# Kernel optimization log

Hardware: AMD Instinct MI355X
Metric: run time of the kernel (lower is better)

## Reference

```python
import jax, jax.numpy as jnp
import numpy as np

HEADS = 8
KD = 64  # key_dim
VD = 64  # value_dim


def _conv1x1(W, b, x):
    # 1x1 conv == per-pixel matmul over channels. W: [out, in], x: [b, in, h, w]
    return jnp.einsum('oc,bchw->bohw', W, x) + b[:, None, None]


def setup_inputs() -> dict:
    key = jax.random.key(0)
    ks = jax.random.split(key, 9)
    B, C, H, W = 4, 128, 128, 128
    s = 0.02
    return {
        'x':  jax.random.normal(ks[0], (B, C, H, W), jnp.float32),
        'Wq': jax.random.normal(ks[1], (KD * HEADS, C), jnp.float32) * s,
        'bq': jax.random.normal(ks[2], (KD * HEADS,), jnp.float32) * s,
        'Wk': jax.random.normal(ks[3], (KD * HEADS, C), jnp.float32) * s,
        'bk': jax.random.normal(ks[4], (KD * HEADS,), jnp.float32) * s,
        'Wv': jax.random.normal(ks[5], (VD * HEADS, C), jnp.float32) * s,
        'bv': jax.random.normal(ks[6], (VD * HEADS,), jnp.float32) * s,
        'Wo': jax.random.normal(ks[7], (C, VD * HEADS), jnp.float32) * s,
        'bo': jax.random.normal(ks[8], (C,), jnp.float32) * s,
    }


def reference(x, Wq, bq, Wk, bk, Wv, bv, Wo, bo):
    B, C, H, W = x.shape
    n = H * W
    scale = KD ** -0.25
    # projections -> [b, heads, dim, n]
    q = _conv1x1(Wq, bq, x).reshape(B, HEADS, KD, n) * scale
    k = _conv1x1(Wk, bk, x).reshape(B, HEADS, KD, n) * scale
    v = _conv1x1(Wv, bv, x).reshape(B, HEADS, VD, n)
    # linear attention: softmax k over tokens (n), softmax q over key dim (d)
    k = jax.nn.softmax(k, axis=-1)
    q = jax.nn.softmax(q, axis=-2)
    ctx = jnp.einsum('bhdn,bhen->bhde', k, v)   # [b, h, kd, vd] small context
    out = jnp.einsum('bhdn,bhde->bhen', q, ctx)  # [b, h, vd, n]
    out = out.reshape(B, HEADS * VD, H, W)
    return _conv1x1(Wo, bo, out)
```

## Files before the change

### kernel.cpp

```cpp
#include <hip/hip_runtime.h>

typedef unsigned short u16;
typedef __bf16 bf16x8 __attribute__((ext_vector_type(8)));
typedef float f32x4 __attribute__((ext_vector_type(4)));

#define N_ 16384
#define SCALE 0.35355339059327379f

__device__ __forceinline__ u16 f2bf(float f){
  union { float f; unsigned int i; } v; v.f = f;
  unsigned int b = v.i;
  return (u16)((b + 0x7FFFu + ((b >> 16) & 1u)) >> 16);
}
__device__ __forceinline__ unsigned int cvtpk(float a, float b){
  unsigned int r;
  asm("v_cvt_pk_bf16_f32 %0, %1, %2" : "=v"(r) : "v"(a), "v"(b));
  return r;
}

__global__ __launch_bounds__(256) void pconvx(const float* __restrict__ x,
    u16* __restrict__ xt, const float* __restrict__ Wq,
    const float* __restrict__ bq, const float* __restrict__ Wk,
    const float* __restrict__ bk, const float* __restrict__ Wv,
    const float* __restrict__ bv, u16* __restrict__ wkvf, u16* __restrict__ wqf,
    float* __restrict__ bkv, float* __restrict__ bqs){
  const int tid = threadIdx.x;
  const int bid = blockIdx.x;
  if (bid < 512){
    const int b = bid >> 7;
    const int kq = tid >> 6;
    const int t0 = (bid & 127) * 128 + 2 * (tid & 63);
    const float* xp = x + (size_t)(b * 128 + kq * 32) * N_ + t0;
    u16* dst = xt + (size_t)(b * N_ + t0) * 128;
#pragma unroll
    for (int gi = 0; gi < 4; gi++){
      float2 v[8];
#pragma unroll
      for (int j = 0; j < 8; j++)
        v[j] = *(const float2*)(xp + (size_t)(gi * 8 + j) * N_);
      const int g = kq * 4 + gi;
      {
        uint4 o;
        o.x = cvtpk(v[0].x, v[1].x); o.y = cvtpk(v[2].x, v[3].x);
        o.z = cvtpk(v[4].x, v[5].x); o.w = cvtpk(v[6].x, v[7].x);
        *(uint4*)(dst + ((g ^ (t0 & 15)) * 8)) = o;
      }
      {
        uint4 o;
        o.x = cvtpk(v[0].y, v[1].y); o.y = cvtpk(v[2].y, v[3].y);
        o.z = cvtpk(v[4].y, v[5].y); o.w = cvtpk(v[6].y, v[7].y);
        const int t = t0 + 1;
        *(uint4*)(dst + 128 + ((g ^ (t & 15)) * 8)) = o;
      }
    }
    return;
  }
  const int T = (bid - 512) * 256 + tid;
  if (T < 1024){
    int jj = T & 127, h = T >> 7;
    bkv[T] = (jj < 64) ? SCALE * bk[h * 64 + jj] : bv[h * 64 + jj - 64];
  } else if (T < 1536){
    bqs[T - 1024] = SCALE * bq[T - 1024];
  }
  const float* src; float sc; u16* dst;
  if (T < 16384){
    int l = T & 63, f = T >> 6;
    int ks = f & 3, jt = (f >> 2) & 7, h = f >> 5;
    int jj = 16 * jt + (l & 15);
    int k0 = ks * 32 + (l >> 4) * 8;
    if (jj < 64){ src = Wk + (size_t)(h * 64 + jj) * 128 + k0; sc = SCALE; }
    else        { src = Wv + (size_t)(h * 64 + jj - 64) * 128 + k0; sc = 1.f; }
    dst = wkvf + (size_t)f * 512 + l * 8;
  } else {
    int T2 = T - 16384;
    int l = T2 & 63, f = T2 >> 6;
    int ks = f & 3, dt = (f >> 2) & 3, h = f >> 4;
    int d = 16 * dt + (l & 15);
    int k0 = ks * 32 + (l >> 4) * 8;
    src = Wq + (size_t)(h * 64 + d) * 128 + k0; sc = SCALE;
    dst = wqf + (size_t)f * 512 + l * 8;
  }
  float4 a = *(const float4*)src, c = *(const float4*)(src + 4);
  ushort4 o0, o1;
  o0.x = f2bf(sc * a.x); o0.y = f2bf(sc * a.y); o0.z = f2bf(sc * a.z); o0.w = f2bf(sc * a.w);
  o1.x = f2bf(sc * c.x); o1.y = f2bf(sc * c.y); o1.z = f2bf(sc * c.z); o1.w = f2bf(sc * c.w);
  *(ushort4*)dst = o0; *(ushort4*)(dst + 4) = o1;
}

__global__ __launch_bounds__(256, 2) void kvctx(const u16* __restrict__ xt,
    const u16* __restrict__ wkvf, const float* __restrict__ bkv,
    float* __restrict__ pctx, float* __restrict__ prs){
  __shared__ u16 smem[32768];
  const int tid = threadIdx.x;
  const int chunk = blockIdx.x, h = blockIdx.y, b = blockIdx.z;
  const int w = tid >> 6, l = tid & 63, r15 = l & 15, q = l >> 4;
  const int th = w & 1, jh = w >> 1;

  bf16x8 wf[4][4];
#pragma unroll
  for (int ni = 0; ni < 4; ni++)
#pragma unroll
    for (int ks = 0; ks < 4; ks++)
      wf[ni][ks] = *(const bf16x8*)(wkvf +
          (size_t)((h * 8 + 4 * jh + ni) * 4 + ks) * 512 + l * 8);
  float barr[4];
#pragma unroll
  for (int ni = 0; ni < 4; ni++)
    barr[ni] = bkv[h * 128 + jh * 64 + 16 * ni + r15];

  const size_t tok0 = (size_t)b * N_ + chunk * 512;
  const char* gbase = (const char*)(xt + tok0 * 128);
  u16* sekv = smem + 16384;

#define STAGE(sub_)                                                            \
  {                                                                            \
    const char* gs = gbase + (size_t)(sub_)*32768 + w * 8192 + l * 16;         \
    char* ls = (char*)smem + w * 8192;                                         \
    _Pragma("unroll")                                                          \
    for (int p = 0; p < 8; p++)                                                \
      __builtin_amdgcn_global_load_lds(                                        \
          (const __attribute__((address_space(1))) void*)(gs + p * 1024),      \
          (__attribute__((address_space(3))) void*)(ls + p * 1024), 16, 0, 0); \
  }

  STAGE(0);
  __syncthreads();

  f32x4 acc2[4][4] = {};
  float rs[4] = {0.f, 0.f, 0.f, 0.f};

  for (int sub = 0; sub < 4; sub++){
    f32x4 acc1[4][4] = {};
#pragma unroll
    for (int ks = 0; ks < 4; ks++){
      bf16x8 xa[4];
#pragma unroll
      for (int mi = 0; mi < 4; mi++){
        int t = th * 64 + 16 * mi + r15;
        xa[mi] = *(const bf16x8*)&smem[t * 128 + (((ks * 4 + q) ^ r15) * 8)];
      }
#pragma unroll
      for (int mi = 0; mi < 4; mi++)
#pragma unroll
        for (int ni = 0; ni < 4; ni++)
          acc1[mi][ni] = __builtin_amdgcn_mfma_f32_16x16x32_bf16(
              xa[mi], wf[ni][ks], acc1[mi][ni], 0, 0, 0);
    }
    asm volatile("s_waitcnt lgkmcnt(0)" ::: "memory");
    __builtin_amdgcn_s_barrier();
    if (sub < 3) STAGE(sub + 1);
#pragma unroll
    for (int ni = 0; ni < 4; ni++){
      const float bb = barr[ni];
      const int j = jh * 64 + 16 * ni + r15;
      float ps = 0.f;
#pragma unroll
      for (int mi = 0; mi < 4; mi++){
        float vals[4];
#pragma unroll
        for (int r = 0; r < 4; r++) vals[r] = acc1[mi][ni][r] + bb;
        if (jh == 0){
#pragma unroll
          for (int r = 0; r < 4; r++){ vals[r] = __expf(vals[r]); ps += vals[r]; }
        }
        uint2 pk;
        pk.x = cvtpk(vals[0], vals[1]);
        pk.y = cvtpk(vals[2], vals[3]);
        int g8 = 16 * th + 4 * mi + q;
        int g8s = g8 ^ (2 * r15);
        *(uint2*)&sekv[j * 128 + g8s * 4] = pk;
      }
      if (jh == 0){
        ps += __shfl_xor(ps, 16); ps += __shfl_xor(ps, 32);
        rs[ni] += ps;
      }
    }
    asm volatile("s_waitcnt lgkmcnt(0)" ::: "memory");
    __builtin_amdgcn_s_barrier();
    {
      bf16x8 ka[4], va[4];
      const int g8s = (8 * w + 2 * q) ^ (2 * r15);
#pragma unroll
      for (int mi2 = 0; mi2 < 4; mi2++){
        int d = 16 * mi2 + r15;
        ka[mi2] = *(const bf16x8*)&sekv[d * 128 + g8s * 4];
      }
#pragma unroll
      for (int ni2 = 0; ni2 < 4; ni2++){
        int e = 16 * ni2 + r15;
        va[ni2] = *(const bf16x8*)&sekv[(64 + e) * 128 + g8s * 4];
      }
#pragma unroll
      for (int mi2 = 0; mi2 < 4; mi2++)
#pragma unroll
        for (int ni2 = 0; ni2 < 4; ni2++)
          acc2[mi2][ni2] = __builtin_amdgcn_mfma_f32_16x16x32_bf16(
              ka[mi2], va[ni2], acc2[mi2][ni2], 0, 0, 0);
    }
    __syncthreads();
  }
#undef STAGE
  float* fb = (float*)smem;
#pragma unroll
  for (int mi2 = 0; mi2 < 4; mi2++)
#pragma unroll
    for (int ni2 = 0; ni2 < 4; ni2++)
#pragma unroll
      for (int r = 0; r < 4; r++){
        int d = 16 * mi2 + 4 * q + r, e = 16 * ni2 + r15;
        fb[w * 4096 + d * 64 + e] = acc2[mi2][ni2][r];
      }
  __syncthreads();
  {
    float* dst = pctx + ((size_t)((b * 8 + h) * 32 + chunk)) * 4096 + tid * 16;
#pragma unroll
    for (int i = 0; i < 4; i++){
      int o = tid * 16 + 4 * i;
      float4 a = *(const float4*)(fb + o);
      float4 c = *(const float4*)(fb + 4096 + o);
      float4 d = *(const float4*)(fb + 8192 + o);
      float4 e = *(const float4*)(fb + 12288 + o);
      float4 s;
      s.x = a.x + c.x + d.x + e.x; s.y = a.y + c.y + d.y + e.y;
      s.z = a.z + c.z + d.z + e.z; s.w = a.w + c.w + d.w + e.w;
      *(float4*)(dst + 4 * i) = s;
    }
  }
  if (jh == 0 && q == 0){
    float* rb = prs + ((size_t)((b * 8 + h) * 32 + chunk)) * 128 + th * 64;
#pragma unroll
    for (int ni = 0; ni < 4; ni++) rb[16 * ni + r15] = rs[ni];
  }
}

__global__ __launch_bounds__(256) void redmker(const float* __restrict__ pctx,
    const float* __restrict__ prs, const float* __restrict__ Wo,
    u16* __restrict__ mtf){
  __shared__ float ctxh8[8][68];
  __shared__ float woht[64][132];
  __shared__ float rsh[8];
  const int tid = threadIdx.x;
  const int bh = blockIdx.x, s = blockIdx.y;
  const int h = bh & 7;
  {
    const int e4 = tid & 15, r0 = tid >> 4;
#pragma unroll
    for (int p = 0; p < 8; p++){
      int c = r0 + p * 16;
      float4 v = *(const float4*)(Wo + (size_t)c * 512 + h * 64 + 4 * e4);
      woht[4 * e4 + 0][c] = v.x; woht[4 * e4 + 1][c] = v.y;
      woht[4 * e4 + 2][c] = v.z; woht[4 * e4 + 3][c] = v.w;
    }
  }
  {
    const float* base = pctx + (size_t)bh * 131072 + s * 512 + tid * 2;
    float2 a = {0.f, 0.f};
#pragma unroll 4
    for (int c = 0; c < 32; c++){
      float2 v = *(const float2*)(base + c * 4096);
      a.x += v.x; a.y += v.y;
    }
    const int i = tid * 2;
    ctxh8[i >> 6][i & 63] = a.x;
    ctxh8[(i + 1) >> 6][(i + 1) & 63] = a.y;
  }
  {
    const int dl = tid >> 5, c = tid & 31;
    const int dg = s * 8 + dl;
    const float* rb = prs + (size_t)bh * 4096 + c * 128;
    float v = rb[dg] + rb[64 + dg];
    v += __shfl_xor(v, 1);  v += __shfl_xor(v, 2);
    v += __shfl_xor(v, 4);  v += __shfl_xor(v, 8);
    v += __shfl_xor(v, 16);
    if (c == 0) rsh[dl] = v;
  }
  __syncthreads();
  const int dl = tid >> 5, c0 = (tid & 31) * 4;
  const int d = s * 8 + dl;
  const float inv = 1.f / rsh[dl];
  float acc[4] = {0.f, 0.f, 0.f, 0.f};
  for (int e = 0; e < 64; e++){
    float cv = ctxh8[dl][e];
#pragma unroll
    for (int j = 0; j < 4; j++) acc[j] += cv * woht[e][c0 + j];
  }
  const int ks = d >> 5, lq = ((d >> 3) & 3) << 4, el = d & 7;
#pragma unroll
  for (int j = 0; j < 4; j++){
    int c = c0 + j;
    mtf[((size_t)(bh * 8 + (c >> 4)) * 2 + ks) * 512 + ((c & 15) | lq) * 8 + el]
        = f2bf(inv * acc[j]);
  }
}

__global__ __launch_bounds__(256, 3) void qout(const u16* __restrict__ xt,
    const u16* __restrict__ wqf, const float* __restrict__ bqs,
    const u16* __restrict__ mtf, const float* __restrict__ bo,
    float* __restrict__ out){
  __shared__ u16 smP[4][16 * 64];
  const int tid = threadIdx.x;
  const int tt = blockIdx.x, b = blockIdx.y;
  const int w = tid >> 6, l = tid & 63, r15 = l & 15, q = l >> 4;
  const int t0 = tt * 64;
  const int m7 = 2 * (r15 & 7);
  const int t = t0 + w * 16 + r15;

  bf16x8 xb[4];
#pragma unroll
  for (int ks = 0; ks < 4; ks++)
    xb[ks] = *(const bf16x8*)(xt + (size_t)(b * N_ + t) * 128 +
                              (((ks * 4 + q) ^ r15) * 8));

  u16* sp = smP[w];
  f32x4 acc3[8] = {};
  for (int h = 0; h < 8; h++){
    float bq_[4][4];
#pragma unroll
    for (int mi = 0; mi < 4; mi++){
      float4 v = *(const float4*)(bqs + h * 64 + 16 * mi + 4 * q);
      bq_[mi][0] = v.x; bq_[mi][1] = v.y; bq_[mi][2] = v.z; bq_[mi][3] = v.w;
    }
    f32x4 acc1[4] = {};
#pragma unroll
    for (int ks = 0; ks < 4; ks++){
      bf16x8 wqv[4];
#pragma unroll
      for (int mi = 0; mi < 4; mi++)
        wqv[mi] = *(const bf16x8*)(wqf +
            (size_t)((h * 4 + mi) * 4 + ks) * 512 + l * 8);
#pragma unroll
      for (int mi = 0; mi < 4; mi++)
        acc1[mi] = __builtin_amdgcn_mfma_f32_16x16x32_bf16(
            wqv[mi], xb[ks], acc1[mi], 0, 0, 0);
    }
    bf16x8 mfA[4], mfB[4];
#pragma unroll
    for (int mm = 0; mm < 4; mm++)
      mfA[mm] = *(const bf16x8*)(mtf +
          ((size_t)((b * 8 + h) * 8 + mm) * 2 + 0) * 512 + l * 8);
#pragma unroll
    for (int mm = 0; mm < 4; mm++)
      mfB[mm] = *(const bf16x8*)(mtf +
          ((size_t)((b * 8 + h) * 8 + 4 + mm) * 2 + 0) * 512 + l * 8);
    {
      float ps = 0.f;
#pragma unroll
      for (int mi = 0; mi < 4; mi++)
#pragma unroll
        for (int r = 0; r < 4; r++){
          float e = __expf(acc1[mi][r] + bq_[mi][r]);
          acc1[mi][r] = e; ps += e;
        }
      ps += __shfl_xor(ps, 16); ps += __shfl_xor(ps, 32);
      const float ci = 1.f / ps;
#pragma unroll
      for (int mi = 0; mi < 4; mi++){
        uint2 pk;
        pk.x = cvtpk(acc1[mi][0] * ci, acc1[mi][1] * ci);
        pk.y = cvtpk(acc1[mi][2] * ci, acc1[mi][3] * ci);
        int g8s = (4 * mi + q) ^ m7;
        *(uint2*)&sp[r15 * 64 + g8s * 4] = pk;
      }
    }
    bf16x8 pb0 = *(const bf16x8*)&sp[r15 * 64 + (((2 * q) ^ m7) * 4)];
    bf16x8 pb1 = *(const bf16x8*)&sp[r15 * 64 + (((8 + 2 * q) ^ m7) * 4)];
#pragma unroll
    for (int mm = 0; mm < 4; mm++)
      acc3[mm] = __builtin_amdgcn_mfma_f32_16x16x32_bf16(
          mfA[mm], pb0, acc3[mm], 0, 0, 0);
#pragma unroll
    for (int mm = 0; mm < 4; mm++)
      mfA[mm] = *(const bf16x8*)(mtf +
          ((size_t)((b * 8 + h) * 8 + mm) * 2 + 1) * 512 + l * 8);
#pragma unroll
    for (int mm = 0; mm < 4; mm++)
      acc3[4 + mm] = __builtin_amdgcn_mfma_f32_16x16x32_bf16(
          mfB[mm], pb0, acc3[4 + mm], 0, 0, 0);
#pragma unroll
    for (int mm = 0; mm < 4; mm++)
      mfB[mm] = *(const bf16x8*)(mtf +
          ((size_t)((b * 8 + h) * 8 + 4 + mm) * 2 + 1) * 512 + l * 8);
#pragma unroll
    for (int mm = 0; mm < 4; mm++)
      acc3[mm] = __builtin_amdgcn_mfma_f32_16x16x32_bf16(
          mfA[mm], pb1, acc3[mm], 0, 0, 0);
#pragma unroll
    for (int mm = 0; mm < 4; mm++)
      acc3[4 + mm] = __builtin_amdgcn_mfma_f32_16x16x32_bf16(
          mfB[mm], pb1, acc3[4 + mm], 0, 0, 0);
  }
#pragma unroll
  for (int mi = 0; mi < 8; mi++){
    float4 bv = *(const float4*)(bo + 16 * mi + 4 * q);
    float bs[4] = {bv.x, bv.y, bv.z, bv.w};
#pragma unroll
    for (int r = 0; r < 4; r++){
      int c = 16 * mi + 4 * q + r;
      out[(size_t)(b * 128 + c) * N_ + t] = acc3[mi][r] + bs[r];
    }
  }
}

extern "C" void kernel_launch(void* const* d_in, const int* in_sizes, int n_in,
                              void* d_out, int out_size, void* d_ws, size_t ws_size,
                              hipStream_t stream){
  const float* x  = (const float*)d_in[0];
  const float* Wq = (const float*)d_in[1];
  const float* bq = (const float*)d_in[2];
  const float* Wk = (const float*)d_in[3];
  const float* bk = (const float*)d_in[4];
  const float* Wv = (const float*)d_in[5];
  const float* bv = (const float*)d_in[6];
  const float* Wo = (const float*)d_in[7];
  const float* bo = (const float*)d_in[8];
  float* out = (float*)d_out;

  char* ws = (char*)d_ws;
  u16*   xt     = (u16*)ws;
  u16*   wkvf   = (u16*)(ws + 16777216);
  u16*   wqf    = (u16*)(ws + 17039360);
  u16*   mtf    = (u16*)(ws + 17170432);
  float* bkv    = (float*)(ws + 17694720);
  float* bqs    = (float*)(ws + 17698816);
  float* pctx   = (float*)(ws + 18233344);
  float* prs    = (float*)(ws + 35010560);

  pconvx <<<608, 256, 0, stream>>>(x, xt, Wq, bq, Wk, bk, Wv, bv,
                                   wkvf, wqf, bkv, bqs);
  kvctx  <<<dim3(32, 8, 4), 256, 0, stream>>>(xt, wkvf, bkv, pctx, prs);
  redmker<<<dim3(32, 8), 256, 0, stream>>>(pctx, prs, Wo, mtf);
  qout   <<<dim3(256, 4), 256, 0, stream>>>(xt, wqf, bqs, mtf, bo, out);
}
```

Before: 192.0 us.

## Double-buffer per-head mtf tiles into LDS via async global_load_lds in qout

Each head's 16KB output-projection tile (mtf) is now staged into a double-buffered shared-memory array using global_load_lds, with the next head's tile prefetched while the current head computes. Previously every wave loaded these fragments straight from global memory, duplicated across the four waves of a block. The change cuts redundant global traffic and overlaps loading with compute, but adds 32KB of LDS per block, which may lower occupancy below the 3-blocks hint, plus a barrier per head.

```diff
diff --git a/kernel.cpp b/kernel.cpp
--- a/kernel.cpp
+++ b/kernel.cpp
@@ -297,6 +297,7 @@
     const u16* __restrict__ wqf, const float* __restrict__ bqs,
     const u16* __restrict__ mtf, const float* __restrict__ bo,
     float* __restrict__ out){
+  __shared__ u16 smM[2][8192];
   __shared__ u16 smP[4][16 * 64];
   const int tid = threadIdx.x;
   const int tt = blockIdx.x, b = blockIdx.y;
@@ -305,15 +306,32 @@
   const int m7 = 2 * (r15 & 7);
   const int t = t0 + w * 16 + r15;
 
+#define STAGEM(h_, bb_)                                                        \
+  {                                                                            \
+    const char* gs = (const char*)(mtf + (size_t)(b * 8 + (h_)) * 8192) +      \
+                     w * 4096 + l * 16;                                        \
+    char* ls = (char*)smM[bb_] + w * 4096;                                     \
+    _Pragma("unroll")                                                          \
+    for (int p = 0; p < 4; p++)                                                \
+      __builtin_amdgcn_global_load_lds(                                        \
+          (const __attribute__((address_space(1))) void*)(gs + p * 1024),      \
+          (__attribute__((address_space(3))) void*)(ls + p * 1024), 16, 0, 0); \
+  }
+
   bf16x8 xb[4];
 #pragma unroll
   for (int ks = 0; ks < 4; ks++)
     xb[ks] = *(const bf16x8*)(xt + (size_t)(b * N_ + t) * 128 +
                               (((ks * 4 + q) ^ r15) * 8));
 
+  STAGEM(0, 0);
+  __syncthreads();
+
   u16* sp = smP[w];
   f32x4 acc3[8] = {};
   for (int h = 0; h < 8; h++){
+    const int buf = h & 1;
+    if (h < 7) STAGEM(h + 1, buf ^ 1);
     float bq_[4][4];
 #pragma unroll
     for (int mi = 0; mi < 4; mi++){
@@ -333,15 +351,6 @@
         acc1[mi] = __builtin_amdgcn_mfma_f32_16x16x32_bf16(
             wqv[mi], xb[ks], acc1[mi], 0, 0, 0);
     }
-    bf16x8 mfA[4], mfB[4];
-#pragma unroll
-    for (int mm = 0; mm < 4; mm++)
-      mfA[mm] = *(const bf16x8*)(mtf +
-          ((size_t)((b * 8 + h) * 8 + mm) * 2 + 0) * 512 + l * 8);
-#pragma unroll
-    for (int mm = 0; mm < 4; mm++)
-      mfB[mm] = *(const bf16x8*)(mtf +
-          ((size_t)((b * 8 + h) * 8 + 4 + mm) * 2 + 0) * 512 + l * 8);
     {
       float ps = 0.f;
 #pragma unroll
@@ -362,33 +371,20 @@
         *(uint2*)&sp[r15 * 64 + g8s * 4] = pk;
       }
     }
-    bf16x8 pb0 = *(const bf16x8*)&sp[r15 * 64 + (((2 * q) ^ m7) * 4)];
-    bf16x8 pb1 = *(const bf16x8*)&sp[r15 * 64 + (((8 + 2 * q) ^ m7) * 4)];
-#pragma unroll
-    for (int mm = 0; mm < 4; mm++)
-      acc3[mm] = __builtin_amdgcn_mfma_f32_16x16x32_bf16(
-          mfA[mm], pb0, acc3[mm], 0, 0, 0);
-#pragma unroll
-    for (int mm = 0; mm < 4; mm++)
-      mfA[mm] = *(const bf16x8*)(mtf +
-          ((size_t)((b * 8 + h) * 8 + mm) * 2 + 1) * 512 + l * 8);
-#pragma unroll
-    for (int mm = 0; mm < 4; mm++)
-      acc3[4 + mm] = __builtin_amdgcn_mfma_f32_16x16x32_bf16(
-          mfB[mm], pb0, acc3[4 + mm], 0, 0, 0);
-#pragma unroll
-    for (int mm = 0; mm < 4; mm++)
-      mfB[mm] = *(const bf16x8*)(mtf +
-          ((size_t)((b * 8 + h) * 8 + 4 + mm) * 2 + 1) * 512 + l * 8);
-#pragma unroll
-    for (int mm = 0; mm < 4; mm++)
-      acc3[mm] = __builtin_amdgcn_mfma_f32_16x16x32_bf16(
-          mfA[mm], pb1, acc3[mm], 0, 0, 0);
-#pragma unroll
-    for (int mm = 0; mm < 4; mm++)
-      acc3[4 + mm] = __builtin_amdgcn_mfma_f32_16x16x32_bf16(
-          mfB[mm], pb1, acc3[4 + mm], 0, 0, 0);
-  }
+#pragma unroll
+    for (int ks2 = 0; ks2 < 2; ks2++){
+      const int g8s = (8 * ks2 + 2 * q) ^ m7;
+      bf16x8 pb = *(const bf16x8*)&sp[r15 * 64 + g8s * 4];
+#pragma unroll
+      for (int mm = 0; mm < 8; mm++){
+        bf16x8 mf = *(const bf16x8*)&smM[buf][(mm * 2 + ks2) * 512 + l * 8];
+        acc3[mm] = __builtin_amdgcn_mfma_f32_16x16x32_bf16(
+            mf, pb, acc3[mm], 0, 0, 0);
+      }
+    }
+    if (h < 7) __syncthreads();
+  }
+#undef STAGEM
 #pragma unroll
   for (int mi = 0; mi < 8; mi++){
     float4 bv = *(const float4*)(bo + 16 * mi + 4 * q);
```

After: 191.8 us. No clear change (-0.1%).

## Fuse four kernels into one cooperative persistent kernel with grid syncs

Applied to the files above, without the earlier changes.

Replaces the four separate launches (convert/pack, kv context, reduce, q+output) with one cooperative kernel of 512 blocks that runs each stage in turn, separated by grid-wide syncs. Blocks loop over work items when a stage has more units than the grid. The aim is to remove per-launch overhead and the gaps between kernels. In exchange, the 64KB shared buffer and 2-blocks-per-CU bound limit occupancy, and the stages with fewer work units leave blocks idle at each grid barrier. If the cooperative launch fails, it falls back to the old four launches.

```diff
diff --git a/kernel.cpp b/kernel.cpp
--- a/kernel.cpp
+++ b/kernel.cpp
@@ -1,4 +1,7 @@
 #include <hip/hip_runtime.h>
+#include <hip/hip_cooperative_groups.h>
+
+namespace cg = cooperative_groups;
 
 typedef unsigned short u16;
 typedef __bf16 bf16x8 __attribute__((ext_vector_type(8)));
@@ -16,6 +19,396 @@
   unsigned int r;
   asm("v_cvt_pk_bf16_f32 %0, %1, %2" : "=v"(r) : "v"(a), "v"(b));
   return r;
+}
+
+__global__ __launch_bounds__(256, 2) void fused(
+    const float* __restrict__ x,  const float* __restrict__ Wq,
+    const float* __restrict__ bq, const float* __restrict__ Wk,
+    const float* __restrict__ bk, const float* __restrict__ Wv,
+    const float* __restrict__ bv, const float* __restrict__ Wo,
+    const float* __restrict__ bo, float* __restrict__ out,
+    u16* __restrict__ xt, u16* __restrict__ wkvf, u16* __restrict__ wqf,
+    u16* __restrict__ mtf, float* __restrict__ bkv, float* __restrict__ bqs,
+    float* __restrict__ pctx, float* __restrict__ prs)
+{
+  __shared__ __align__(16) char SM[65536];
+  const int bid = blockIdx.x;
+  const int tid = threadIdx.x;
+
+  {
+    const int b = bid >> 7;
+    const int kq = tid >> 6;
+    const int t0 = (bid & 127) * 128 + 2 * (tid & 63);
+    const float* xp = x + (size_t)(b * 128 + kq * 32) * N_ + t0;
+    u16* dst = xt + (size_t)(b * N_ + t0) * 128;
+#pragma unroll
+    for (int gi = 0; gi < 4; gi++){
+      float2 v[8];
+#pragma unroll
+      for (int j = 0; j < 8; j++)
+        v[j] = *(const float2*)(xp + (size_t)(gi * 8 + j) * N_);
+      const int g = kq * 4 + gi;
+      {
+        uint4 o;
+        o.x = cvtpk(v[0].x, v[1].x); o.y = cvtpk(v[2].x, v[3].x);
+        o.z = cvtpk(v[4].x, v[5].x); o.w = cvtpk(v[6].x, v[7].x);
+        *(uint4*)(dst + ((g ^ (t0 & 15)) * 8)) = o;
+      }
+      {
+        uint4 o;
+        o.x = cvtpk(v[0].y, v[1].y); o.y = cvtpk(v[2].y, v[3].y);
+        o.z = cvtpk(v[4].y, v[5].y); o.w = cvtpk(v[6].y, v[7].y);
+        const int t = t0 + 1;
+        *(uint4*)(dst + 128 + ((g ^ (t & 15)) * 8)) = o;
+      }
+    }
+  }
+  if (bid < 96){
+    const int T = bid * 256 + tid;
+    if (T < 1024){
+      int jj = T & 127, h = T >> 7;
+      bkv[T] = (jj < 64) ? SCALE * bk[h * 64 + jj] : bv[h * 64 + jj - 64];
+    } else if (T < 1536){
+      bqs[T - 1024] = SCALE * bq[T - 1024];
+    }
+    const float* src; float sc; u16* dst;
+    if (T < 16384){
+      int l = T & 63, f = T >> 6;
+      int ks = f & 3, jt = (f >> 2) & 7, h = f >> 5;
+      int jj = 16 * jt + (l & 15);
+      int k0 = ks * 32 + (l >> 4) * 8;
+      if (jj < 64){ src = Wk + (size_t)(h * 64 + jj) * 128 + k0; sc = SCALE; }
+      else        { src = Wv + (size_t)(h * 64 + jj - 64) * 128 + k0; sc = 1.f; }
+      dst = wkvf + (size_t)f * 512 + l * 8;
+    } else {
+      int T2 = T - 16384;
+      int l = T2 & 63, f = T2 >> 6;
+      int ks = f & 3, dt = (f >> 2) & 3, h = f >> 4;
+      int d = 16 * dt + (l & 15);
+      int k0 = ks * 32 + (l >> 4) * 8;
+      src = Wq + (size_t)(h * 64 + d) * 128 + k0; sc = SCALE;
+      dst = wqf + (size_t)f * 512 + l * 8;
+    }
+    float4 a = *(const float4*)src, c = *(const float4*)(src + 4);
+    ushort4 o0, o1;
+    o0.x = f2bf(sc * a.x); o0.y = f2bf(sc * a.y); o0.z = f2bf(sc * a.z); o0.w = f2bf(sc * a.w);
+    o1.x = f2bf(sc * c.x); o1.y = f2bf(sc * c.y); o1.z = f2bf(sc * c.z); o1.w = f2bf(sc * c.w);
+    *(ushort4*)dst = o0; *(ushort4*)(dst + 4) = o1;
+  }
+  __threadfence();
+  cg::this_grid().sync();
+
+  {
+    u16* smem = (u16*)SM;
+    const int w = tid >> 6, l = tid & 63, r15 = l & 15, q = l >> 4;
+    const int th = w & 1, jh = w >> 1;
+    for (int u = bid; u < 1024; u += 512){
+      const int chunk = u & 31, h = (u >> 5) & 7, b = u >> 8;
+      __syncthreads();
+
+      bf16x8 wf[4][4];
+#pragma unroll
+      for (int ni = 0; ni < 4; ni++)
+#pragma unroll
+        for (int ks = 0; ks < 4; ks++)
+          wf[ni][ks] = *(const bf16x8*)(wkvf +
+              (size_t)((h * 8 + 4 * jh + ni) * 4 + ks) * 512 + l * 8);
+      float barr[4];
+#pragma unroll
+      for (int ni = 0; ni < 4; ni++)
+        barr[ni] = bkv[h * 128 + jh * 64 + 16 * ni + r15];
+
+      const size_t tok0 = (size_t)b * N_ + chunk * 512;
+      const char* gbase = (const char*)(xt + tok0 * 128);
+      u16* sekv = smem + 16384;
+
+#define STAGE(sub_)                                                            \
+  {                                                                            \
+    const char* gs = gbase + (size_t)(sub_)*32768 + w * 8192 + l * 16;         \
+    char* ls = (char*)smem + w * 8192;                                         \
+    _Pragma("unroll")                                                          \
+    for (int p = 0; p < 8; p++)                                                \
+      __builtin_amdgcn_global_load_lds(                                        \
+          (const __attribute__((address_space(1))) void*)(gs + p * 1024),      \
+          (__attribute__((address_space(3))) void*)(ls + p * 1024), 16, 0, 0); \
+  }
+
+      STAGE(0);
+      __syncthreads();
+
+      f32x4 acc2[4][4] = {};
+      float rs[4] = {0.f, 0.f, 0.f, 0.f};
+
+      for (int sub = 0; sub < 4; sub++){
+        f32x4 acc1[4][4] = {};
+#pragma unroll
+        for (int ks = 0; ks < 4; ks++){
+          bf16x8 xa[4];
+#pragma unroll
+          for (int mi = 0; mi < 4; mi++){
+            int t = th * 64 + 16 * mi + r15;
+            xa[mi] = *(const bf16x8*)&smem[t * 128 + (((ks * 4 + q) ^ r15) * 8)];
+          }
+#pragma unroll
+          for (int mi = 0; mi < 4; mi++)
+#pragma unroll
+            for (int ni = 0; ni < 4; ni++)
+              acc1[mi][ni] = __builtin_amdgcn_mfma_f32_16x16x32_bf16(
+                  xa[mi], wf[ni][ks], acc1[mi][ni], 0, 0, 0);
+        }
+        asm volatile("s_waitcnt lgkmcnt(0)" ::: "memory");
+        __builtin_amdgcn_s_barrier();
+        if (sub < 3) STAGE(sub + 1);
+#pragma unroll
+        for (int ni = 0; ni < 4; ni++){
+          const float bb = barr[ni];
+          const int j = jh * 64 + 16 * ni + r15;
+          float ps = 0.f;
+#pragma unroll
+          for (int mi = 0; mi < 4; mi++){
+            float vals[4];
+#pragma unroll
+            for (int r = 0; r < 4; r++) vals[r] = acc1[mi][ni][r] + bb;
+            if (jh == 0){
+#pragma unroll
+              for (int r = 0; r < 4; r++){ vals[r] = __expf(vals[r]); ps += vals[r]; }
+            }
+            uint2 pk;
+            pk.x = cvtpk(vals[0], vals[1]);
+            pk.y = cvtpk(vals[2], vals[3]);
+            int g8 = 16 * th + 4 * mi + q;
+            int g8s = g8 ^ (2 * r15);
+            *(uint2*)&sekv[j * 128 + g8s * 4] = pk;
+          }
+          if (jh == 0){
+            ps += __shfl_xor(ps, 16); ps += __shfl_xor(ps, 32);
+            rs[ni] += ps;
+          }
+        }
+        asm volatile("s_waitcnt lgkmcnt(0)" ::: "memory");
+        __builtin_amdgcn_s_barrier();
+        {
+          bf16x8 ka[4], va[4];
+          const int g8s = (8 * w + 2 * q) ^ (2 * r15);
+#pragma unroll
+          for (int mi2 = 0; mi2 < 4; mi2++){
+            int d = 16 * mi2 + r15;
+            ka[mi2] = *(const bf16x8*)&sekv[d * 128 + g8s * 4];
+          }
+#pragma unroll
+          for (int ni2 = 0; ni2 < 4; ni2++){
+            int e = 16 * ni2 + r15;
+            va[ni2] = *(const bf16x8*)&sekv[(64 + e) * 128 + g8s * 4];
+          }
+#pragma unroll
+          for (int mi2 = 0; mi2 < 4; mi2++)
+#pragma unroll
+            for (int ni2 = 0; ni2 < 4; ni2++)
+              acc2[mi2][ni2] = __builtin_amdgcn_mfma_f32_16x16x32_bf16(
+                  ka[mi2], va[ni2], acc2[mi2][ni2], 0, 0, 0);
+        }
+        __syncthreads();
+      }
+#undef STAGE
+      float* fb = (float*)smem;
+#pragma unroll
+      for (int mi2 = 0; mi2 < 4; mi2++)
+#pragma unroll
+        for (int ni2 = 0; ni2 < 4; ni2++)
+#pragma unroll
+          for (int r = 0; r < 4; r++){
+            int d = 16 * mi2 + 4 * q + r, e = 16 * ni2 + r15;
+            fb[w * 4096 + d * 64 + e] = acc2[mi2][ni2][r];
+          }
+      __syncthreads();
+      {
+        float* dst = pctx + ((size_t)((b * 8 + h) * 32 + chunk)) * 4096 + tid * 16;
+#pragma unroll
+        for (int i = 0; i < 4; i++){
+          int o = tid * 16 + 4 * i;
+          float4 a = *(const float4*)(fb + o);
+          float4 c = *(const float4*)(fb + 4096 + o);
+          float4 d = *(const float4*)(fb + 8192 + o);
+          float4 e = *(const float4*)(fb + 12288 + o);
+          float4 s;
+          s.x = a.x + c.x + d.x + e.x; s.y = a.y + c.y + d.y + e.y;
+          s.z = a.z + c.z + d.z + e.z; s.w = a.w + c.w + d.w + e.w;
+          *(float4*)(dst + 4 * i) = s;
+        }
+      }
+      if (jh == 0 && q == 0){
+        float* rb = prs + ((size_t)((b * 8 + h) * 32 + chunk)) * 128 + th * 64;
+#pragma unroll
+        for (int ni = 0; ni < 4; ni++) rb[16 * ni + r15] = rs[ni];
+      }
+    }
+  }
+  __threadfence();
+  cg::this_grid().sync();
+
+  if (bid < 256){
+    const int bh = bid & 31, s = bid >> 5;
+    const int h = bh & 7;
+    float* ctxh8 = (float*)SM;
+    float* woht  = (float*)(SM + 2176);
+    float* rsh   = (float*)(SM + 2176 + 33792);
+    {
+      const int e4 = tid & 15, r0 = tid >> 4;
+#pragma unroll
+      for (int p = 0; p < 8; p++){
+        int c = r0 + p * 16;
+        float4 v = *(const float4*)(Wo + (size_t)c * 512 + h * 64 + 4 * e4);
+        woht[(4 * e4 + 0) * 132 + c] = v.x; woht[(4 * e4 + 1) * 132 + c] = v.y;
+        woht[(4 * e4 + 2) * 132 + c] = v.z; woht[(4 * e4 + 3) * 132 + c] = v.w;
+      }
+    }
+    {
+      const float* base = pctx + (size_t)bh * 131072 + s * 512 + tid * 2;
+      float2 a = {0.f, 0.f};
+#pragma unroll 4
+      for (int c = 0; c < 32; c++){
+        float2 v = *(const float2*)(base + c * 4096);
+        a.x += v.x; a.y += v.y;
+      }
+      const int i = tid * 2;
+      ctxh8[(i >> 6) * 68 + (i & 63)] = a.x;
+      ctxh8[((i + 1) >> 6) * 68 + ((i + 1) & 63)] = a.y;
+    }
+    {
+      const int dl = tid >> 5, c = tid & 31;
+      const int dg = s * 8 + dl;
+      const float* rb = prs + (size_t)bh * 4096 + c * 128;
+      float v = rb[dg] + rb[64 + dg];
+      v += __shfl_xor(v, 1);  v += __shfl_xor(v, 2);
+      v += __shfl_xor(v, 4);  v += __shfl_xor(v, 8);
+      v += __shfl_xor(v, 16);
+      if (c == 0) rsh[dl] = v;
+    }
+    __syncthreads();
+    const int dl = tid >> 5, c0 = (tid & 31) * 4;
+    const int d = s * 8 + dl;
+    const float inv = 1.f / rsh[dl];
+    float acc[4] = {0.f, 0.f, 0.f, 0.f};
+    for (int e = 0; e < 64; e++){
+      float cv = ctxh8[dl * 68 + e];
+#pragma unroll
+      for (int j = 0; j < 4; j++) acc[j] += cv * woht[e * 132 + c0 + j];
+    }
+    const int ks = d >> 5, lq = ((d >> 3) & 3) << 4, el = d & 7;
+#pragma unroll
+    for (int j = 0; j < 4; j++){
+      int c = c0 + j;
+      mtf[((size_t)(bh * 8 + (c >> 4)) * 2 + ks) * 512 + ((c & 15) | lq) * 8 + el]
+          = f2bf(inv * acc[j]);
+    }
+  }
+  __threadfence();
+  cg::this_grid().sync();
+
+  {
+    const int w = tid >> 6, l = tid & 63, r15 = l & 15, q = l >> 4;
+    const int m7 = 2 * (r15 & 7);
+    u16* sp = (u16*)SM + w * 1024;
+    for (int u = bid; u < 1024; u += 512){
+      const int tt = u & 255, b = u >> 8;
+      const int t0 = tt * 64;
+      const int t = t0 + w * 16 + r15;
+
+      bf16x8 xb[4];
+#pragma unroll
+      for (int ks = 0; ks < 4; ks++)
+        xb[ks] = *(const bf16x8*)(xt + (size_t)(b * N_ + t) * 128 +
+                                  (((ks * 4 + q) ^ r15) * 8));
+
+      f32x4 acc3[8] = {};
+      for (int h = 0; h < 8; h++){
+        float bq_[4][4];
+#pragma unroll
+        for (int mi = 0; mi < 4; mi++){
+          float4 v = *(const float4*)(bqs + h * 64 + 16 * mi + 4 * q);
+          bq_[mi][0] = v.x; bq_[mi][1] = v.y; bq_[mi][2] = v.z; bq_[mi][3] = v.w;
+        }
+        f32x4 acc1[4] = {};
+#pragma unroll
+        for (int ks = 0; ks < 4; ks++){
+          bf16x8 wqv[4];
+#pragma unroll
+          for (int mi = 0; mi < 4; mi++)
+            wqv[mi] = *(const bf16x8*)(wqf +
+                (size_t)((h * 4 + mi) * 4 + ks) * 512 + l * 8);
+#pragma unroll
+          for (int mi = 0; mi < 4; mi++)
+            acc1[mi] = __builtin_amdgcn_mfma_f32_16x16x32_bf16(
+                wqv[mi], xb[ks], acc1[mi], 0, 0, 0);
+        }
+        bf16x8 mfA[4], mfB[4];
+#pragma unroll
+        for (int mm = 0; mm < 4; mm++)
+          mfA[mm] = *(const bf16x8*)(mtf +
+              ((size_t)((b * 8 + h) * 8 + mm) * 2 + 0) * 512 + l * 8);
+#pragma unroll
+        for (int mm = 0; mm < 4; mm++)
+          mfB[mm] = *(const bf16x8*)(mtf +
+              ((size_t)((b * 8 + h) * 8 + 4 + mm) * 2 + 0) * 512 + l * 8);
+        {
+          float ps = 0.f;
+#pragma unroll
+          for (int mi = 0; mi < 4; mi++)
+#pragma unroll
+            for (int r = 0; r < 4; r++){
+              float e = __expf(acc1[mi][r] + bq_[mi][r]);
+              acc1[mi][r] = e; ps += e;
+            }
+          ps += __shfl_xor(ps, 16); ps += __shfl_xor(ps, 32);
+          const float ci = 1.f / ps;
+#pragma unroll
+          for (int mi = 0; mi < 4; mi++){
+            uint2 pk;
+            pk.x = cvtpk(acc1[mi][0] * ci, acc1[mi][1] * ci);
+            pk.y = cvtpk(acc1[mi][2] * ci, acc1[mi][3] * ci);
+            int g8s = (4 * mi + q) ^ m7;
+            *(uint2*)&sp[r15 * 64 + g8s * 4] = pk;
+          }
+        }
+        bf16x8 pb0 = *(const bf16x8*)&sp[r15 * 64 + (((2 * q) ^ m7) * 4)];
+        bf16x8 pb1 = *(const bf16x8*)&sp[r15 * 64 + (((8 + 2 * q) ^ m7) * 4)];
+#pragma unroll
+        for (int mm = 0; mm < 4; mm++)
+          acc3[mm] = __builtin_amdgcn_mfma_f32_16x16x32_bf16(
+              mfA[mm], pb0, acc3[mm], 0, 0, 0);
+#pragma unroll
+        for (int mm = 0; mm < 4; mm++)
+          mfA[mm] = *(const bf16x8*)(mtf +
+              ((size_t)((b * 8 + h) * 8 + mm) * 2 + 1) * 512 + l * 8);
+#pragma unroll
+        for (int mm = 0; mm < 4; mm++)
+          acc3[4 + mm] = __builtin_amdgcn_mfma_f32_16x16x32_bf16(
+              mfB[mm], pb0, acc3[4 + mm], 0, 0, 0);
+#pragma unroll
+        for (int mm = 0; mm < 4; mm++)
+          mfB[mm] = *(const bf16x8*)(mtf +
+              ((size_t)((b * 8 + h) * 8 + 4 + mm) * 2 + 1) * 512 + l * 8);
+#pragma unroll
+        for (int mm = 0; mm < 4; mm++)
+          acc3[mm] = __builtin_amdgcn_mfma_f32_16x16x32_bf16(
+              mfA[mm], pb1, acc3[mm], 0, 0, 0);
+#pragma unroll
+        for (int mm = 0; mm < 4; mm++)
+          acc3[4 + mm] = __builtin_amdgcn_mfma_f32_16x16x32_bf16(
+              mfB[mm], pb1, acc3[4 + mm], 0, 0, 0);
+      }
+#pragma unroll
+      for (int mi = 0; mi < 8; mi++){
+        float4 bv = *(const float4*)(bo + 16 * mi + 4 * q);
+        float bs[4] = {bv.x, bv.y, bv.z, bv.w};
+#pragma unroll
+        for (int r = 0; r < 4; r++){
+          int c = 16 * mi + 4 * q + r;
+          out[(size_t)(b * 128 + c) * N_ + t] = acc3[mi][r] + bs[r];
+        }
+      }
+    }
+  }
 }
 
 __global__ __launch_bounds__(256) void pconvx(const float* __restrict__ x,
@@ -425,9 +818,19 @@
   float* pctx   = (float*)(ws + 18233344);
   float* prs    = (float*)(ws + 35010560);
 
-  pconvx <<<608, 256, 0, stream>>>(x, xt, Wq, bq, Wk, bk, Wv, bv,
-                                   wkvf, wqf, bkv, bqs);
-  kvctx  <<<dim3(32, 8, 4), 256, 0, stream>>>(xt, wkvf, bkv, pctx, prs);
-  redmker<<<dim3(32, 8), 256, 0, stream>>>(pctx, prs, Wo, mtf);
-  qout   <<<dim3(256, 4), 256, 0, stream>>>(xt, wqf, bqs, mtf, bo, out);
+  void* args[] = {
+    (void*)&x, (void*)&Wq, (void*)&bq, (void*)&Wk, (void*)&bk,
+    (void*)&Wv, (void*)&bv, (void*)&Wo, (void*)&bo, (void*)&out,
+    (void*)&xt, (void*)&wkvf, (void*)&wqf, (void*)&mtf,
+    (void*)&bkv, (void*)&bqs, (void*)&pctx, (void*)&prs
+  };
+  hipError_t err = hipLaunchCooperativeKernel(
+      (void*)fused, dim3(512), dim3(256), args, 0, stream);
+  if (err != hipSuccess){
+    pconvx <<<608, 256, 0, stream>>>(x, xt, Wq, bq, Wk, bk, Wv, bv,
+                                     wkvf, wqf, bkv, bqs);
+    kvctx  <<<dim3(32, 8, 4), 256, 0, stream>>>(xt, wkvf, bkv, pctx, prs);
+    redmker<<<dim3(32, 8), 256, 0, stream>>>(pctx, prs, Wo, mtf);
+    qout   <<<dim3(256, 4), 256, 0, stream>>>(xt, wqf, bqs, mtf, bo, out);
+  }
 }
```

Result: slower. 590.6 us (+207.7%).

## Halve kvctx sub-tile size, split context GEMM per wave, raise occupancy

Applied to the files above, without the earlier changes.

Each staged token sub-tile in kvctx shrinks from 128 to 64 tokens, with twice as many iterations, which halves LDS use. The kernel also stops holding the K/V weight fragments in registers and reloads them from global memory every k-step. The second GEMM is now split so each wave owns a distinct 32x32 quadrant of the 64x64 context, so the cross-wave reduction through LDS goes away and results are written straight to global memory. Launch bounds rise to 4 blocks per SM to raise occupancy, at the cost of repeated weight loads and more barriers per token.

```diff
diff --git a/kernel.cpp b/kernel.cpp
--- a/kernel.cpp
+++ b/kernel.cpp
@@ -87,22 +87,17 @@
   *(ushort4*)dst = o0; *(ushort4*)(dst + 4) = o1;
 }
 
-__global__ __launch_bounds__(256, 2) void kvctx(const u16* __restrict__ xt,
+__global__ __launch_bounds__(256, 4) void kvctx(const u16* __restrict__ xt,
     const u16* __restrict__ wkvf, const float* __restrict__ bkv,
     float* __restrict__ pctx, float* __restrict__ prs){
-  __shared__ u16 smem[32768];
+  __shared__ u16 smem[16384];
   const int tid = threadIdx.x;
   const int chunk = blockIdx.x, h = blockIdx.y, b = blockIdx.z;
   const int w = tid >> 6, l = tid & 63, r15 = l & 15, q = l >> 4;
   const int th = w & 1, jh = w >> 1;
-
-  bf16x8 wf[4][4];
-#pragma unroll
-  for (int ni = 0; ni < 4; ni++)
-#pragma unroll
-    for (int ks = 0; ks < 4; ks++)
-      wf[ni][ks] = *(const bf16x8*)(wkvf +
-          (size_t)((h * 8 + 4 * jh + ni) * 4 + ks) * 512 + l * 8);
+  const int dw = w & 1, ew = w >> 1;
+  const int sw = r15 & 14;
+
   float barr[4];
 #pragma unroll
   for (int ni = 0; ni < 4; ni++)
@@ -110,14 +105,14 @@
 
   const size_t tok0 = (size_t)b * N_ + chunk * 512;
   const char* gbase = (const char*)(xt + tok0 * 128);
-  u16* sekv = smem + 16384;
+  u16* sekv = smem + 8192;
 
 #define STAGE(sub_)                                                            \
   {                                                                            \
-    const char* gs = gbase + (size_t)(sub_)*32768 + w * 8192 + l * 16;         \
-    char* ls = (char*)smem + w * 8192;                                         \
+    const char* gs = gbase + (size_t)(sub_)*16384 + w * 4096 + l * 16;         \
+    char* ls = (char*)smem + w * 4096;                                         \
     _Pragma("unroll")                                                          \
-    for (int p = 0; p < 8; p++)                                                \
+    for (int p = 0; p < 4; p++)                                                \
       __builtin_amdgcn_global_load_lds(                                        \
           (const __attribute__((address_space(1))) void*)(gs + p * 1024),      \
           (__attribute__((address_space(3))) void*)(ls + p * 1024), 16, 0, 0); \
@@ -126,36 +121,41 @@
   STAGE(0);
   __syncthreads();
 
-  f32x4 acc2[4][4] = {};
+  f32x4 acc2[2][2] = {};
   float rs[4] = {0.f, 0.f, 0.f, 0.f};
 
-  for (int sub = 0; sub < 4; sub++){
-    f32x4 acc1[4][4] = {};
+  for (int sub = 0; sub < 8; sub++){
+    f32x4 acc1[2][4] = {};
 #pragma unroll
     for (int ks = 0; ks < 4; ks++){
-      bf16x8 xa[4];
-#pragma unroll
-      for (int mi = 0; mi < 4; mi++){
-        int t = th * 64 + 16 * mi + r15;
+      bf16x8 wfv[4];
+#pragma unroll
+      for (int ni = 0; ni < 4; ni++)
+        wfv[ni] = *(const bf16x8*)(wkvf +
+            (size_t)((h * 8 + 4 * jh + ni) * 4 + ks) * 512 + l * 8);
+      bf16x8 xa[2];
+#pragma unroll
+      for (int mi = 0; mi < 2; mi++){
+        int t = th * 32 + 16 * mi + r15;
         xa[mi] = *(const bf16x8*)&smem[t * 128 + (((ks * 4 + q) ^ r15) * 8)];
       }
 #pragma unroll
-      for (int mi = 0; mi < 4; mi++)
+      for (int mi = 0; mi < 2; mi++)
 #pragma unroll
         for (int ni = 0; ni < 4; ni++)
           acc1[mi][ni] = __builtin_amdgcn_mfma_f32_16x16x32_bf16(
-              xa[mi], wf[ni][ks], acc1[mi][ni], 0, 0, 0);
+              xa[mi], wfv[ni], acc1[mi][ni], 0, 0, 0);
     }
     asm volatile("s_waitcnt lgkmcnt(0)" ::: "memory");
     __builtin_amdgcn_s_barrier();
-    if (sub < 3) STAGE(sub + 1);
+    if (sub < 7) STAGE(sub + 1);
 #pragma unroll
     for (int ni = 0; ni < 4; ni++){
       const float bb = barr[ni];
       const int j = jh * 64 + 16 * ni + r15;
       float ps = 0.f;
 #pragma unroll
-      for (int mi = 0; mi < 4; mi++){
+      for (int mi = 0; mi < 2; mi++){
         float vals[4];
 #pragma unroll
         for (int r = 0; r < 4; r++) vals[r] = acc1[mi][ni][r] + bb;
@@ -166,9 +166,9 @@
         uint2 pk;
         pk.x = cvtpk(vals[0], vals[1]);
         pk.y = cvtpk(vals[2], vals[3]);
-        int g8 = 16 * th + 4 * mi + q;
-        int g8s = g8 ^ (2 * r15);
-        *(uint2*)&sekv[j * 128 + g8s * 4] = pk;
+        int g8 = 8 * th + 4 * mi + q;
+        int g8s = g8 ^ sw;
+        *(uint2*)&sekv[j * 64 + g8s * 4] = pk;
       }
       if (jh == 0){
         ps += __shfl_xor(ps, 16); ps += __shfl_xor(ps, 32);
@@ -177,54 +177,33 @@
     }
     asm volatile("s_waitcnt lgkmcnt(0)" ::: "memory");
     __builtin_amdgcn_s_barrier();
-    {
-      bf16x8 ka[4], va[4];
-      const int g8s = (8 * w + 2 * q) ^ (2 * r15);
-#pragma unroll
-      for (int mi2 = 0; mi2 < 4; mi2++){
-        int d = 16 * mi2 + r15;
-        ka[mi2] = *(const bf16x8*)&sekv[d * 128 + g8s * 4];
-      }
-#pragma unroll
-      for (int ni2 = 0; ni2 < 4; ni2++){
-        int e = 16 * ni2 + r15;
-        va[ni2] = *(const bf16x8*)&sekv[(64 + e) * 128 + g8s * 4];
-      }
-#pragma unroll
-      for (int mi2 = 0; mi2 < 4; mi2++)
-#pragma unroll
-        for (int ni2 = 0; ni2 < 4; ni2++)
-          acc2[mi2][ni2] = __builtin_amdgcn_mfma_f32_16x16x32_bf16(
-              ka[mi2], va[ni2], acc2[mi2][ni2], 0, 0, 0);
+#pragma unroll
+    for (int ks2 = 0; ks2 < 2; ks2++){
+      const int gr = ((8 * ks2 + 2 * q) ^ sw) * 4;
+      bf16x8 ka0 = *(const bf16x8*)&sekv[(32 * dw + r15) * 64 + gr];
+      bf16x8 ka1 = *(const bf16x8*)&sekv[(32 * dw + 16 + r15) * 64 + gr];
+      bf16x8 va0 = *(const bf16x8*)&sekv[(64 + 32 * ew + r15) * 64 + gr];
+      bf16x8 va1 = *(const bf16x8*)&sekv[(64 + 32 * ew + 16 + r15) * 64 + gr];
+      acc2[0][0] = __builtin_amdgcn_mfma_f32_16x16x32_bf16(ka0, va0, acc2[0][0], 0, 0, 0);
+      acc2[0][1] = __builtin_amdgcn_mfma_f32_16x16x32_bf16(ka0, va1, acc2[0][1], 0, 0, 0);
+      acc2[1][0] = __builtin_amdgcn_mfma_f32_16x16x32_bf16(ka1, va0, acc2[1][0], 0, 0, 0);
+      acc2[1][1] = __builtin_amdgcn_mfma_f32_16x16x32_bf16(ka1, va1, acc2[1][1], 0, 0, 0);
     }
     __syncthreads();
   }
 #undef STAGE
-  float* fb = (float*)smem;
-#pragma unroll
-  for (int mi2 = 0; mi2 < 4; mi2++)
-#pragma unroll
-    for (int ni2 = 0; ni2 < 4; ni2++)
-#pragma unroll
-      for (int r = 0; r < 4; r++){
-        int d = 16 * mi2 + 4 * q + r, e = 16 * ni2 + r15;
-        fb[w * 4096 + d * 64 + e] = acc2[mi2][ni2][r];
-      }
-  __syncthreads();
   {
-    float* dst = pctx + ((size_t)((b * 8 + h) * 32 + chunk)) * 4096 + tid * 16;
-#pragma unroll
-    for (int i = 0; i < 4; i++){
-      int o = tid * 16 + 4 * i;
-      float4 a = *(const float4*)(fb + o);
-      float4 c = *(const float4*)(fb + 4096 + o);
-      float4 d = *(const float4*)(fb + 8192 + o);
-      float4 e = *(const float4*)(fb + 12288 + o);
-      float4 s;
-      s.x = a.x + c.x + d.x + e.x; s.y = a.y + c.y + d.y + e.y;
-      s.z = a.z + c.z + d.z + e.z; s.w = a.w + c.w + d.w + e.w;
-      *(float4*)(dst + 4 * i) = s;
-    }
+    float* dst = pctx + ((size_t)((b * 8 + h) * 32 + chunk)) * 4096;
+#pragma unroll
+    for (int df = 0; df < 2; df++)
+#pragma unroll
+      for (int ef = 0; ef < 2; ef++)
+#pragma unroll
+        for (int r = 0; r < 4; r++){
+          int d = 32 * dw + 16 * df + 4 * q + r;
+          int e = 32 * ew + 16 * ef + r15;
+          dst[d * 64 + e] = acc2[df][ef][r];
+        }
   }
   if (jh == 0 && q == 0){
     float* rb = prs + ((size_t)((b * 8 + h) * 32 + chunk)) * 128 + th * 64;
```

Measured after the change: 221.2 us. 1.15x slower.
